# Optimization experiments

Measured on AMD Instinct MI355X. Metric: run time of the kernel, lower is better.

The kernel has to match this reference:

```python
import jax, jax.numpy as jnp
import numpy as np
import math

C = 8  # sparsity factor c from __init__


def setup_inputs() -> dict:
    key = jax.random.key(0)
    kq, kk, kv, ki = jax.random.split(key, 4)
    B, Q, KV, D = 4, 2048, 2048, 512
    U = int(Q * math.log(KV))  # 15615 sampled keys, matches torch _sampler
    q = jax.random.normal(kq, (B, Q, D), dtype=jnp.float32)
    k = jax.random.normal(kk, (B, KV, D), dtype=jnp.float32)
    v = jax.random.normal(kv, (B, KV, D), dtype=jnp.float32)
    sample_idx = jax.random.randint(ki, (B, U), 0, KV)  # per-batch random key sample
    return {"q": q, "k": k, "v": v, "sample_idx": sample_idx}


def reference(q, k, v, sample_idx):
    B, Q, D = q.shape
    KV = k.shape[1]
    u = int(C * math.log(Q))  # number of selected queries (== 60 here)

    # _sampler: gather sampled keys per batch -> (B, U, D)
    k_bar = jnp.take_along_axis(k, sample_idx[:, :, None], axis=1)

    # sparsity measure M = max_j s_bar - mean_j s_bar, s_bar: (B, Q, U)
    s_bar = jnp.einsum('bqd,bud->bqu', q, k_bar)
    M = s_bar.max(axis=2) - s_bar.mean(axis=2)  # (B, Q)

    # top-u queries per batch
    _, top_idx = jax.lax.top_k(M, u)  # (B, u)
    q_bar = jnp.take_along_axis(q, top_idx[:, :, None], axis=1)  # (B, u, D)

    # small dense attention over full keys; NOTE: original scales by sqrt(kv_len)
    attn = jnp.einsum('bud,bkd->buk', q_bar, k) / jnp.sqrt(jnp.asarray(KV, q.dtype))
    attn = jax.nn.softmax(attn, axis=-1)
    s1 = jnp.einsum('buk,bkd->bud', attn, v)  # (B, u, D)

    # fill all positions with mean of v, then scatter attention outputs
    s = jnp.broadcast_to(v.mean(axis=1, keepdims=True), q.shape)  # (B, Q, D)
    bidx = jnp.arange(B)[:, None]
    s = s.at[bidx, top_idx].set(s1)
    return s
```

## Files before the change

### kernel.cpp

```cpp
#include <hip/hip_runtime.h>
#include <math.h>

#define BATCH 4
#define QN    2048
#define KVN   2048
#define DN    512
#define U_TOT 15615
#define NSEL  60
#define NSLOT 32
#define S1KS  32

typedef __attribute__((ext_vector_type(8))) short bf16x8;
typedef __attribute__((ext_vector_type(4))) float f32x4;

__device__ __forceinline__ unsigned short f2bf(float f) {
  unsigned u = __float_as_uint(f);
  unsigned r = (u + 0x7fffu + ((u >> 16) & 1u)) >> 16;
  return (unsigned short)r;
}
__device__ __forceinline__ float bf2f(unsigned short h) {
  return __uint_as_float(((unsigned)h) << 16);
}
__device__ __forceinline__ void gld16(const void* g, void* l) {
  __builtin_amdgcn_global_load_lds(
      (const __attribute__((address_space(1))) unsigned int*)g,
      (__attribute__((address_space(3))) unsigned int*)l, 16, 0, 0);
}

__global__ __launch_bounds__(256) void pre_kernel(
    const float* __restrict__ q, const float* __restrict__ k,
    const float* __restrict__ v, const int* __restrict__ sidx,
    unsigned short* __restrict__ qhi, unsigned short* __restrict__ qlo,
    unsigned short* __restrict__ khi, unsigned short* __restrict__ klo,
    float* __restrict__ cnt, float* __restrict__ vmean_raw)
{
  __shared__ int h[KVN];
  const int bid = blockIdx.x;
  const int t = threadIdx.x;

  if (bid < 8192) {
    const int half = bid >> 12;
    const int i = (bid & 4095) * 256 + t;
    const float* in = half ? k : q;
    unsigned short* hi = half ? khi : qhi;
    unsigned short* lo = half ? klo : qlo;
    float4 f = reinterpret_cast<const float4*>(in)[i];
    ushort4 hh, ll;
    hh.x = f2bf(f.x); ll.x = f2bf(f.x - bf2f(hh.x));
    hh.y = f2bf(f.y); ll.y = f2bf(f.y - bf2f(hh.y));
    hh.z = f2bf(f.z); ll.z = f2bf(f.z - bf2f(hh.z));
    hh.w = f2bf(f.w); ll.w = f2bf(f.w - bf2f(hh.w));
    reinterpret_cast<ushort4*>(hi)[i] = hh;
    reinterpret_cast<ushort4*>(lo)[i] = ll;
  } else if (bid < 8196) {
    const int b = bid - 8192;
    for (int i = t; i < KVN; i += 256) h[i] = 0;
    __syncthreads();
    for (int i = t; i < U_TOT; i += 256) atomicAdd(&h[sidx[b * U_TOT + i]], 1);
    __syncthreads();
    for (int i = t; i < KVN; i += 256) cnt[b * KVN + i] = (float)h[i];
  } else {
    const int idx = bid - 8196;
    const int b = idx >> 4, ch = idx & 15;
    const float* vb = v + ((size_t)(b * KVN) + ch * 128) * DN;
    float s0 = 0.f, s1 = 0.f;
    for (int r = 0; r < 128; ++r) {
      s0 += vb[(size_t)r * DN + t];
      s1 += vb[(size_t)r * DN + t + 256];
    }
    atomicAdd(&vmean_raw[b * DN + t], s0);
    atomicAdd(&vmean_raw[b * DN + t + 256], s1);
  }
}

#define BAR() asm volatile("s_barrier" ::: "memory")

#define PHASE_MFMA(P) \
  __builtin_amdgcn_s_setprio(1); \
  _Pragma("unroll") \
  for (int n = 0; n < 4; ++n) { \
    acc[2*(P)][n]   = __builtin_amdgcn_mfma_f32_16x16x32_bf16(a0h, bh_[n], acc[2*(P)][n], 0, 0, 0); \
    acc[2*(P)][n]   = __builtin_amdgcn_mfma_f32_16x16x32_bf16(a0h, bl_[n], acc[2*(P)][n], 0, 0, 0); \
    acc[2*(P)][n]   = __builtin_amdgcn_mfma_f32_16x16x32_bf16(a0l, bh_[n], acc[2*(P)][n], 0, 0, 0); \
    acc[2*(P)+1][n] = __builtin_amdgcn_mfma_f32_16x16x32_bf16(a1h, bh_[n], acc[2*(P)+1][n], 0, 0, 0); \
    acc[2*(P)+1][n] = __builtin_amdgcn_mfma_f32_16x16x32_bf16(a1h, bl_[n], acc[2*(P)+1][n], 0, 0, 0); \
    acc[2*(P)+1][n] = __builtin_amdgcn_mfma_f32_16x16x32_bf16(a1l, bh_[n], acc[2*(P)+1][n], 0, 0, 0); \
  } \
  __builtin_amdgcn_s_setprio(0);

#define LOAD_A(P, CB) \
  a0h = *reinterpret_cast<const bf16x8*>(&Ah[CB][(4*(P)+wr)*512 + fr8]); \
  a0l = *reinterpret_cast<const bf16x8*>(&Al[CB][(4*(P)+wr)*512 + fr8]); \
  a1h = *reinterpret_cast<const bf16x8*>(&Ah[CB][(4*(P)+2+wr)*512 + fr8]); \
  a1l = *reinterpret_cast<const bf16x8*>(&Al[CB][(4*(P)+2+wr)*512 + fr8]);

#define LOAD_B(CB) \
  _Pragma("unroll") \
  for (int n = 0; n < 4; ++n) { \
    bh_[n] = *reinterpret_cast<const bf16x8*>(&Bh[CB][wc*2048 + n*512 + fr8]); \
    bl_[n] = *reinterpret_cast<const bf16x8*>(&Bl[CB][wc*2048 + n*512 + fr8]); \
  }

#define KSTEP_MAIN(CB, NB) { \
  gld16(kh0, &Bh[NB][t*8]); gld16(kh1, &Bh[NB][4096 + t*8]); \
  gld16(kl0, &Bl[NB][t*8]); gld16(kl1, &Bl[NB][4096 + t*8]); \
  gld16(qh0, &Ah[NB][t*8]); gld16(ql0, &Al[NB][t*8]); \
  gld16(qh1, &Ah[NB][4096 + t*8]); gld16(ql1, &Al[NB][4096 + t*8]); \
  kh0 += 32; kh1 += 32; kl0 += 32; kl1 += 32; \
  qh0 += 32; qh1 += 32; ql0 += 32; ql1 += 32; \
  { \
    bf16x8 bh_[4], bl_[4], a0h, a0l, a1h, a1l; \
    LOAD_B(CB) \
    LOAD_A(0, CB) \
    PHASE_MFMA(0) \
    LOAD_A(1, CB) \
    PHASE_MFMA(1) \
    LOAD_A(2, CB) \
    PHASE_MFMA(2) \
    LOAD_A(3, CB) \
    PHASE_MFMA(3) \
  } \
  asm volatile("s_waitcnt vmcnt(0)" ::: "memory"); \
  BAR(); \
}

#define KSTEP_LAST(CB) { \
  bf16x8 bh_[4], bl_[4], a0h, a0l, a1h, a1l; \
  LOAD_B(CB) \
  LOAD_A(0, CB) \
  PHASE_MFMA(0) \
  LOAD_A(1, CB) \
  PHASE_MFMA(1) \
  LOAD_A(2, CB) \
  PHASE_MFMA(2) \
  LOAD_A(3, CB) \
  PHASE_MFMA(3) \
}

__global__ __launch_bounds__(512, 2) void s_mfma_kernel(
    const unsigned short* __restrict__ qh, const unsigned short* __restrict__ ql,
    const unsigned short* __restrict__ kh, const unsigned short* __restrict__ kl,
    const float* __restrict__ cnt, float* __restrict__ Pmax, float* __restrict__ Psum)
{
  __shared__ __align__(16) unsigned short Ah[2][8192];
  __shared__ __align__(16) unsigned short Al[2][8192];
  __shared__ __align__(16) unsigned short Bh[2][8192];
  __shared__ __align__(16) unsigned short Bl[2][8192];
  __shared__ float cnt_s[256];

  const int t = threadIdx.x;
  const int w = t >> 6;
  const int L = t & 63;
  const int lm = L & 15;
  const int wr = w >> 2;
  const int wc = w & 3;

  const int bid = blockIdx.x;
  const int xcd = bid & 7;
  const int idx = bid >> 3;
  const int b   = xcd >> 1;
  const int ji  = (xcd & 1) * 4 + (idx >> 3);
  const int qi  = idx & 7;
  const int j0  = ji * 256;
  const int q0  = qi * 256;

  if (t < 256) cnt_s[t] = cnt[b * KVN + j0 + t];

  const int srow = t >> 2;
  const int schk = (t & 3) ^ ((t >> 3) & 3);
  const int perm = (L >> 4) ^ ((lm >> 1) & 3);
  const int fr8  = (4 * lm + perm) * 8;

  const size_t kof = ((size_t)(b * KVN) + j0 + srow) * DN + (size_t)(schk * 8);
  const size_t qof = ((size_t)(b * QN) + q0 + srow) * DN + (size_t)(schk * 8);
  const unsigned short* kh0 = kh + kof;
  const unsigned short* kh1 = kh0 + (size_t)128 * DN;
  const unsigned short* kl0 = kl + kof;
  const unsigned short* kl1 = kl0 + (size_t)128 * DN;
  const unsigned short* qh0 = qh + qof;
  const unsigned short* qh1 = qh0 + (size_t)128 * DN;
  const unsigned short* ql0 = ql + qof;
  const unsigned short* ql1 = ql0 + (size_t)128 * DN;

  f32x4 acc[8][4];
#pragma unroll
  for (int m = 0; m < 8; ++m)
#pragma unroll
    for (int n = 0; n < 4; ++n) {
      acc[m][n][0] = 0.f; acc[m][n][1] = 0.f;
      acc[m][n][2] = 0.f; acc[m][n][3] = 0.f;
    }

  gld16(kh0, &Bh[0][t*8]); gld16(kh1, &Bh[0][4096 + t*8]);
  gld16(kl0, &Bl[0][t*8]); gld16(kl1, &Bl[0][4096 + t*8]);
  gld16(qh0, &Ah[0][t*8]); gld16(ql0, &Al[0][t*8]);
  gld16(qh1, &Ah[0][4096 + t*8]); gld16(ql1, &Al[0][4096 + t*8]);
  kh0 += 32; kh1 += 32; kl0 += 32; kl1 += 32;
  qh0 += 32; qh1 += 32; ql0 += 32; ql1 += 32;
  asm volatile("s_waitcnt vmcnt(0) lgkmcnt(0)" ::: "memory");
  BAR();

#pragma unroll 1
  for (int it = 0; it < 7; ++it) {
    KSTEP_MAIN(0, 1)
    KSTEP_MAIN(1, 0)
  }
  KSTEP_MAIN(0, 1)
  KSTEP_LAST(1)

  const int slot = ji * 4 + wc;
  const size_t spi = (size_t)(slot * BATCH + b);
  const int rgrp = (L >> 4) * 4;
#pragma unroll
  for (int m = 0; m < 8; ++m) {
    float mx[4] = {-INFINITY, -INFINITY, -INFINITY, -INFINITY};
    float ws[4] = {0.f, 0.f, 0.f, 0.f};
#pragma unroll
    for (int n = 0; n < 4; ++n) {
      const float cw = cnt_s[wc * 64 + n * 16 + lm];
      const bool has = (cw > 0.f);
#pragma unroll
      for (int r = 0; r < 4; ++r) {
        const float v = acc[m][n][r];
        if (has) mx[r] = fmaxf(mx[r], v);
        ws[r] = fmaf(cw, v, ws[r]);
      }
    }
#pragma unroll
    for (int r = 0; r < 4; ++r) {
      float mval = mx[r], sval = ws[r];
#pragma unroll
      for (int o = 1; o < 16; o <<= 1) {
        mval = fmaxf(mval, __shfl_xor(mval, o));
        sval += __shfl_xor(sval, o);
      }
      if (lm == 0) {
        const int qrow = q0 + (2 * m + wr) * 16 + rgrp + r;
        Pmax[spi * QN + qrow] = mval;
        Psum[spi * QN + qrow] = sval;
      }
    }
  }
}

__global__ __launch_bounds__(256) void select_kernel(
    const float* __restrict__ Pmax, const float* __restrict__ Psum,
    int* __restrict__ topidx, int* __restrict__ rowslot)
{
  const int b = blockIdx.x;
  const int t = threadIdx.x;
  unsigned long long key[8];
#pragma unroll
  for (int s = 0; s < 8; ++s) {
    const int qq = s * 256 + t;
    float m = -INFINITY, sm = 0.f;
#pragma unroll 4
    for (int p = 0; p < NSLOT; ++p) {
      m = fmaxf(m, Pmax[((size_t)(p * BATCH + b)) * QN + qq]);
      sm += Psum[((size_t)(p * BATCH + b)) * QN + qq];
    }
    const float Mv = m - sm * (1.0f / (float)U_TOT);
    unsigned u = __float_as_uint(Mv);
    u = (u & 0x80000000u) ? ~u : (u | 0x80000000u);
    key[s] = ((unsigned long long)u << 32) | (unsigned)(QN - qq);
    rowslot[b * QN + qq] = -1;
  }

  __shared__ unsigned hist[256];
  __shared__ unsigned long long pref_s;
  __shared__ unsigned rank_s;
  __shared__ unsigned cnt_s;
  if (t == 0) { pref_s = 0ull; rank_s = NSEL; cnt_s = 0u; }
  __syncthreads();

  for (int level = 7; level >= 0; --level) {
    const int shift = level * 8;
    hist[t] = 0;
    __syncthreads();
    const unsigned long long pref = pref_s;
    const unsigned rank = rank_s;
#pragma unroll
    for (int s = 0; s < 8; ++s) {
      const bool match = (level == 7) || ((key[s] >> (shift + 8)) == pref);
      if (match) atomicAdd(&hist[(unsigned)((key[s] >> shift) & 255u)], 1u);
    }
    __syncthreads();
    if (t < 64) {
      const unsigned h0 = hist[4 * t], h1 = hist[4 * t + 1];
      const unsigned h2 = hist[4 * t + 2], h3 = hist[4 * t + 3];
      const unsigned loc = h0 + h1 + h2 + h3;
      unsigned run = loc;
#pragma unroll
      for (int o = 1; o < 64; o <<= 1) {
        const unsigned oth = (unsigned)__shfl_down((int)run, o);
        if (t + o < 64) run += oth;
      }
      const unsigned suf = run - loc;
      const unsigned c3 = suf, c2 = c3 + h3, c1 = c2 + h2, c0 = c1 + h1;
      int hit = -1; unsigned cgt = 0;
      if      (c3 < rank && rank <= c3 + h3) { hit = 4 * t + 3; cgt = c3; }
      else if (c2 < rank && rank <= c2 + h2) { hit = 4 * t + 2; cgt = c2; }
      else if (c1 < rank && rank <= c1 + h1) { hit = 4 * t + 1; cgt = c1; }
      else if (c0 < rank && rank <= c0 + h0) { hit = 4 * t + 0; cgt = c0; }
      if (hit >= 0) {
        pref_s = ((level == 7) ? 0ull : (pref_s << 8)) | (unsigned long long)(unsigned)hit;
        rank_s = rank - cgt;
      }
    }
    __syncthreads();
  }

  const unsigned long long T = pref_s;
#pragma unroll
  for (int s = 0; s < 8; ++s) {
    if (key[s] >= T) {
      const unsigned pos = atomicAdd(&cnt_s, 1u);
      const int qsel = QN - (int)(key[s] & 0xFFFFFFFFull);
      topidx[b * 64 + pos] = qsel;
      rowslot[b * QN + qsel] = (int)pos;
    }
  }
}

#define SBM 64
#define SBN 32
#define SBK 32
__global__ __launch_bounds__(256) void scores_kernel(
    const float* __restrict__ q, const int* __restrict__ topidx,
    const float* __restrict__ k, float* __restrict__ attn)
{
  __shared__ float a_s[SBK][SBM + 4];
  __shared__ float b_s[SBK][SBN + 4];
  __shared__ int tix_s[64];
  const int t  = threadIdx.x;
  const int tx = t & 7;
  const int ty = t >> 3;
  const int kv0 = blockIdx.x * SBN;
  const int b   = blockIdx.y;
  const float* kb = k + (size_t)b * KVN * DN;

  if (t < 64) tix_s[t] = (t < NSEL) ? topidx[b * 64 + t] : 0;
  __syncthreads();

  float acc[2][4];
#pragma unroll
  for (int i = 0; i < 2; ++i)
#pragma unroll
    for (int j = 0; j < 4; ++j) acc[i][j] = 0.f;

  const int c4 = (t & 7) * 4;
  const int r0 = t >> 3;
  const int srow0 = tix_s[r0];
  const int srow1 = tix_s[r0 + 32];

  for (int d0 = 0; d0 < DN; d0 += SBK) {
#pragma unroll
    for (int rr = 0; rr < 2; ++rr) {
      int row = r0 + rr * 32;
      int srow = rr ? srow1 : srow0;
      float4 av = *reinterpret_cast<const float4*>(q + ((size_t)(b * QN) + srow) * DN + d0 + c4);
      a_s[c4 + 0][row] = av.x; a_s[c4 + 1][row] = av.y;
      a_s[c4 + 2][row] = av.z; a_s[c4 + 3][row] = av.w;
    }
    {
      float4 bv = *reinterpret_cast<const float4*>(kb + (size_t)(kv0 + r0) * DN + d0 + c4);
      b_s[c4 + 0][r0] = bv.x; b_s[c4 + 1][r0] = bv.y;
      b_s[c4 + 2][r0] = bv.z; b_s[c4 + 3][r0] = bv.w;
    }
    __syncthreads();
#pragma unroll
    for (int kk = 0; kk < SBK; ++kk) {
      const float a0 = a_s[kk][ty * 2];
      const float a1 = a_s[kk][ty * 2 + 1];
      float4 bv = *reinterpret_cast<const float4*>(&b_s[kk][tx * 4]);
      float bf[4] = {bv.x, bv.y, bv.z, bv.w};
#pragma unroll
      for (int j = 0; j < 4; ++j) {
        acc[0][j] = fmaf(a0, bf[j], acc[0][j]);
        acc[1][j] = fmaf(a1, bf[j], acc[1][j]);
      }
    }
    __syncthreads();
  }

  const float sc = 0.022097086912079608f;
#pragma unroll
  for (int i = 0; i < 2; ++i) {
    int j = ty * 2 + i;
    if (j < NSEL) {
      float4 o = make_float4(__expf(acc[i][0] * sc), __expf(acc[i][1] * sc),
                             __expf(acc[i][2] * sc), __expf(acc[i][3] * sc));
      *reinterpret_cast<float4*>(attn + ((size_t)(b * NSEL + j)) * KVN + kv0 + tx * 4) = o;
    }
  }
}

__global__ __launch_bounds__(256) void s1_partial_kernel(
    const float* __restrict__ attn, const float* __restrict__ v,
    float* __restrict__ part, float* __restrict__ epart)
{
  __shared__ float a_s[64][61];
  const int t    = threadIdx.x;
  const int dv4  = t & 63;
  const int jg   = t >> 6;
  const int dh   = blockIdx.x;
  const int b    = blockIdx.y;
  const int ks   = blockIdx.z;
  const int kv0  = ks * 64;
  const int dbase = dh * 256 + dv4 * 4;

  for (int x = t; x < NSEL * 64; x += 256) {
    const int j = x >> 6, kk = x & 63;
    a_s[kk][j] = attn[((size_t)(b * NSEL + j)) * KVN + kv0 + kk];
  }
  __syncthreads();

  if (dh == 0 && t < NSEL) {
    float es = 0.f;
    for (int kk = 0; kk < 64; ++kk) es += a_s[kk][t];
    epart[(ks * BATCH + b) * 64 + t] = es;
  }

  f32x4 acc[15];
#pragma unroll
  for (int i = 0; i < 15; ++i) { acc[i][0] = 0.f; acc[i][1] = 0.f; acc[i][2] = 0.f; acc[i][3] = 0.f; }

  const float* vb = v + ((size_t)b * KVN + kv0) * DN + dbase;
#pragma unroll 4
  for (int kk = 0; kk < 64; ++kk) {
    const f32x4 vv = *reinterpret_cast<const f32x4*>(vb + (size_t)kk * DN);
#pragma unroll
    for (int jj = 0; jj < 15; ++jj) {
      const float a = a_s[kk][jg * 15 + jj];
      acc[jj][0] = fmaf(a, vv[0], acc[jj][0]);
      acc[jj][1] = fmaf(a, vv[1], acc[jj][1]);
      acc[jj][2] = fmaf(a, vv[2], acc[jj][2]);
      acc[jj][3] = fmaf(a, vv[3], acc[jj][3]);
    }
  }

#pragma unroll
  for (int jj = 0; jj < 15; ++jj) {
    const int j = jg * 15 + jj;
    *reinterpret_cast<f32x4*>(
        part + ((size_t)((ks * BATCH + b) * NSEL) + j) * DN + dbase) = acc[jj];
  }
}

__global__ __launch_bounds__(256) void out_kernel(
    const float* __restrict__ part, const float* __restrict__ epart,
    const float* __restrict__ vmean_raw, const int* __restrict__ rowslot,
    float* __restrict__ out)
{
  const int gid = blockIdx.x * 256 + threadIdx.x;
  const int d4 = gid & 127;
  const int qq = (gid >> 7) & (QN - 1);
  const int b  = gid >> 18;
  const int slot = rowslot[b * QN + qq];
  f32x4 o;
  if (slot >= 0) {
    o[0] = 0.f; o[1] = 0.f; o[2] = 0.f; o[3] = 0.f;
    float es = 0.f;
    for (int ks = 0; ks < S1KS; ++ks) {
      const f32x4 p = reinterpret_cast<const f32x4*>(part)[
          ((size_t)((ks * BATCH + b) * NSEL) + slot) * (DN / 4) + d4];
      o[0] += p[0]; o[1] += p[1]; o[2] += p[2]; o[3] += p[3];
      es += epart[(ks * BATCH + b) * 64 + slot];
    }
    const float inv = 1.f / es;
    o[0] *= inv; o[1] *= inv; o[2] *= inv; o[3] *= inv;
  } else {
    o = reinterpret_cast<const f32x4*>(vmean_raw)[b * (DN / 4) + d4];
    const float s = 1.0f / (float)KVN;
    o[0] *= s; o[1] *= s; o[2] *= s; o[3] *= s;
  }
  reinterpret_cast<f32x4*>(out)[gid] = o;
}

extern "C" void kernel_launch(void* const* d_in, const int* in_sizes, int n_in,
                              void* d_out, int out_size, void* d_ws, size_t ws_size,
                              hipStream_t stream) {
  const float* q    = (const float*)d_in[0];
  const float* k    = (const float*)d_in[1];
  const float* v    = (const float*)d_in[2];
  const int*   sidx = (const int*)d_in[3];
  float* out = (float*)d_out;
  char*  W   = (char*)d_ws;

  const size_t NEL = (size_t)BATCH * QN * DN;
  unsigned short* qh = (unsigned short*)W;
  unsigned short* ql = qh + NEL;
  unsigned short* kh = ql + NEL;
  unsigned short* kl = kh + NEL;

  char* W2 = W + 37748736;
  float* cnt     = (float*)W2;
  float* Pmax    = (float*)(W2 + 32768);
  float* Psum    = (float*)(W2 + 32768 + 1048576);
  int*   topidx  = (int*)(W2 + 32768 + 2097152 + 32768);
  int*   rowslot = (int*)(W2 + 32768 + 2097152 + 32768 + 4096);

  float* attn  = (float*)W;
  float* part  = (float*)(W + 2097152);
  float* epart = (float*)(W + 33554432);
  float* vmean = (float*)(W + 34078720);

  hipMemsetAsync(vmean, 0, BATCH * DN * sizeof(float), stream);
  pre_kernel<<<dim3(8260), 256, 0, stream>>>(q, k, v, sidx, qh, ql, kh, kl, cnt, vmean);
  s_mfma_kernel<<<dim3(256), 512, 0, stream>>>(qh, ql, kh, kl, cnt, Pmax, Psum);
  select_kernel<<<dim3(BATCH), 256, 0, stream>>>(Pmax, Psum, topidx, rowslot);
  scores_kernel<<<dim3(KVN / SBN, BATCH), 256, 0, stream>>>(q, topidx, k, attn);
  s1_partial_kernel<<<dim3(2, BATCH, S1KS), 256, 0, stream>>>(attn, v, part, epart);
  out_kernel<<<dim3(4096), 256, 0, stream>>>(part, epart, vmean, rowslot, out);
}
```

Before: 238.6 us.

## Fold V mean into s1 partial pass and split preprocessing kernel

Moves the column mean of V out of the preprocessing kernel and computes it inside s1_partial_kernel, which already streams V, writing per-chunk partial sums. A small combine kernel reduces those partials, so the memset and the float atomics go away. The histogram is moved into its own 1024-thread kernel. This saves one full read of V in exchange for two extra kernel launches and a small extra reduction.

```diff
diff --git a/kernel.cpp b/kernel.cpp
--- a/kernel.cpp
+++ b/kernel.cpp
@@ -27,50 +27,36 @@
       (__attribute__((address_space(3))) unsigned int*)l, 16, 0, 0);
 }
 
-__global__ __launch_bounds__(256) void pre_kernel(
+__global__ __launch_bounds__(256) void split_kernel(
     const float* __restrict__ q, const float* __restrict__ k,
-    const float* __restrict__ v, const int* __restrict__ sidx,
     unsigned short* __restrict__ qhi, unsigned short* __restrict__ qlo,
-    unsigned short* __restrict__ khi, unsigned short* __restrict__ klo,
-    float* __restrict__ cnt, float* __restrict__ vmean_raw)
+    unsigned short* __restrict__ khi, unsigned short* __restrict__ klo)
+{
+  const int half = blockIdx.x >> 12;
+  const int i = (blockIdx.x & 4095) * 256 + threadIdx.x;
+  const float* in = half ? k : q;
+  unsigned short* hi = half ? khi : qhi;
+  unsigned short* lo = half ? klo : qlo;
+  float4 f = reinterpret_cast<const float4*>(in)[i];
+  ushort4 h, l;
+  h.x = f2bf(f.x); l.x = f2bf(f.x - bf2f(h.x));
+  h.y = f2bf(f.y); l.y = f2bf(f.y - bf2f(h.y));
+  h.z = f2bf(f.z); l.z = f2bf(f.z - bf2f(h.z));
+  h.w = f2bf(f.w); l.w = f2bf(f.w - bf2f(h.w));
+  reinterpret_cast<ushort4*>(hi)[i] = h;
+  reinterpret_cast<ushort4*>(lo)[i] = l;
+}
+
+__global__ __launch_bounds__(1024) void count_kernel(
+    const int* __restrict__ sidx, float* __restrict__ cnt)
 {
   __shared__ int h[KVN];
-  const int bid = blockIdx.x;
-  const int t = threadIdx.x;
-
-  if (bid < 8192) {
-    const int half = bid >> 12;
-    const int i = (bid & 4095) * 256 + t;
-    const float* in = half ? k : q;
-    unsigned short* hi = half ? khi : qhi;
-    unsigned short* lo = half ? klo : qlo;
-    float4 f = reinterpret_cast<const float4*>(in)[i];
-    ushort4 hh, ll;
-    hh.x = f2bf(f.x); ll.x = f2bf(f.x - bf2f(hh.x));
-    hh.y = f2bf(f.y); ll.y = f2bf(f.y - bf2f(hh.y));
-    hh.z = f2bf(f.z); ll.z = f2bf(f.z - bf2f(hh.z));
-    hh.w = f2bf(f.w); ll.w = f2bf(f.w - bf2f(hh.w));
-    reinterpret_cast<ushort4*>(hi)[i] = hh;
-    reinterpret_cast<ushort4*>(lo)[i] = ll;
-  } else if (bid < 8196) {
-    const int b = bid - 8192;
-    for (int i = t; i < KVN; i += 256) h[i] = 0;
-    __syncthreads();
-    for (int i = t; i < U_TOT; i += 256) atomicAdd(&h[sidx[b * U_TOT + i]], 1);
-    __syncthreads();
-    for (int i = t; i < KVN; i += 256) cnt[b * KVN + i] = (float)h[i];
-  } else {
-    const int idx = bid - 8196;
-    const int b = idx >> 4, ch = idx & 15;
-    const float* vb = v + ((size_t)(b * KVN) + ch * 128) * DN;
-    float s0 = 0.f, s1 = 0.f;
-    for (int r = 0; r < 128; ++r) {
-      s0 += vb[(size_t)r * DN + t];
-      s1 += vb[(size_t)r * DN + t + 256];
-    }
-    atomicAdd(&vmean_raw[b * DN + t], s0);
-    atomicAdd(&vmean_raw[b * DN + t + 256], s1);
-  }
+  const int b = blockIdx.x, t = threadIdx.x;
+  for (int i = t; i < KVN; i += 1024) h[i] = 0;
+  __syncthreads();
+  for (int i = t; i < U_TOT; i += 1024) atomicAdd(&h[sidx[b * U_TOT + i]], 1);
+  __syncthreads();
+  for (int i = t; i < KVN; i += 1024) cnt[b * KVN + i] = (float)h[i];
 }
 
 #define BAR() asm volatile("s_barrier" ::: "memory")
@@ -397,7 +383,7 @@
 
 __global__ __launch_bounds__(256) void s1_partial_kernel(
     const float* __restrict__ attn, const float* __restrict__ v,
-    float* __restrict__ part, float* __restrict__ epart)
+    float* __restrict__ part, float* __restrict__ epart, float* __restrict__ vpart)
 {
   __shared__ float a_s[64][61];
   const int t    = threadIdx.x;
@@ -424,11 +410,13 @@
   f32x4 acc[15];
 #pragma unroll
   for (int i = 0; i < 15; ++i) { acc[i][0] = 0.f; acc[i][1] = 0.f; acc[i][2] = 0.f; acc[i][3] = 0.f; }
+  f32x4 vsum; vsum[0] = 0.f; vsum[1] = 0.f; vsum[2] = 0.f; vsum[3] = 0.f;
 
   const float* vb = v + ((size_t)b * KVN + kv0) * DN + dbase;
 #pragma unroll 4
   for (int kk = 0; kk < 64; ++kk) {
     const f32x4 vv = *reinterpret_cast<const f32x4*>(vb + (size_t)kk * DN);
+    if (jg == 0) { vsum[0] += vv[0]; vsum[1] += vv[1]; vsum[2] += vv[2]; vsum[3] += vv[3]; }
 #pragma unroll
     for (int jj = 0; jj < 15; ++jj) {
       const float a = a_s[kk][jg * 15 + jj];
@@ -445,11 +433,24 @@
     *reinterpret_cast<f32x4*>(
         part + ((size_t)((ks * BATCH + b) * NSEL) + j) * DN + dbase) = acc[jj];
   }
+  if (jg == 0)
+    *reinterpret_cast<f32x4*>(vpart + ((size_t)(ks * BATCH + b)) * DN + dbase) = vsum;
+}
+
+__global__ void vmean_combine_kernel(const float* __restrict__ vpart, float* __restrict__ vmean)
+{
+  int idx = blockIdx.x * 256 + threadIdx.x;
+  if (idx < BATCH * DN) {
+    int b = idx / DN, d = idx % DN;
+    float s = 0.f;
+    for (int c = 0; c < S1KS; ++c) s += vpart[(size_t)(c * BATCH + b) * DN + d];
+    vmean[idx] = s * (1.0f / (float)KVN);
+  }
 }
 
 __global__ __launch_bounds__(256) void out_kernel(
     const float* __restrict__ part, const float* __restrict__ epart,
-    const float* __restrict__ vmean_raw, const int* __restrict__ rowslot,
+    const float* __restrict__ vmean, const int* __restrict__ rowslot,
     float* __restrict__ out)
 {
   const int gid = blockIdx.x * 256 + threadIdx.x;
@@ -470,9 +471,7 @@
     const float inv = 1.f / es;
     o[0] *= inv; o[1] *= inv; o[2] *= inv; o[3] *= inv;
   } else {
-    o = reinterpret_cast<const f32x4*>(vmean_raw)[b * (DN / 4) + d4];
-    const float s = 1.0f / (float)KVN;
-    o[0] *= s; o[1] *= s; o[2] *= s; o[3] *= s;
+    o = reinterpret_cast<const f32x4*>(vmean)[b * (DN / 4) + d4];
   }
   reinterpret_cast<f32x4*>(out)[gid] = o;
 }
@@ -502,14 +501,16 @@
 
   float* attn  = (float*)W;
   float* part  = (float*)(W + 2097152);
-  float* epart = (float*)(W + 33554432);
+  float* vpart = (float*)(W + 33554432);
   float* vmean = (float*)(W + 34078720);
-
-  hipMemsetAsync(vmean, 0, BATCH * DN * sizeof(float), stream);
-  pre_kernel<<<dim3(8260), 256, 0, stream>>>(q, k, v, sidx, qh, ql, kh, kl, cnt, vmean);
+  float* epart = (float*)(W + 34209792);
+
+  split_kernel<<<dim3(8192), 256, 0, stream>>>(q, k, qh, ql, kh, kl);
+  count_kernel<<<dim3(BATCH), 1024, 0, stream>>>(sidx, cnt);
   s_mfma_kernel<<<dim3(256), 512, 0, stream>>>(qh, ql, kh, kl, cnt, Pmax, Psum);
   select_kernel<<<dim3(BATCH), 256, 0, stream>>>(Pmax, Psum, topidx, rowslot);
   scores_kernel<<<dim3(KVN / SBN, BATCH), 256, 0, stream>>>(q, topidx, k, attn);
-  s1_partial_kernel<<<dim3(2, BATCH, S1KS), 256, 0, stream>>>(attn, v, part, epart);
+  s1_partial_kernel<<<dim3(2, BATCH, S1KS), 256, 0, stream>>>(attn, v, part, epart, vpart);
+  vmean_combine_kernel<<<dim3(8), 256, 0, stream>>>(vpart, vmean);
   out_kernel<<<dim3(4096), 256, 0, stream>>>(part, epart, vmean, rowslot, out);
 }
```

Result: no change. 238.6 us (+0.0%).
